# Kernel optimization log

Measured on AMD Instinct MI355X. Metric: run time of the kernel, lower is better.

The kernel has to match this reference:

```python
import jax, jax.numpy as jnp
import numpy as np

H = 1024          # hidden_size
C = 4             # residual_channels
RH = 16           # residual_heads
HS = H // RH      # head_size for residual (64)
DR = 8            # delta_rank
M = 4096          # mlp_size
NH = 16           # attention heads
HD = H // NH      # attention head dim (64)
A_SIZE = (C - 1) * RH   # 48
B_SIZE = C * RH         # 64
EPS = 1e-5
SSM_EPS = 1e-5


def rat_read(res, W, gamma, beta, num_outputs):
    # res: [b,l,H*C]; W: [H, num_outputs, C] (Conv1d groups=H)
    b, l, _ = res.shape
    x = res.reshape(b, l, H, C)
    y = jnp.einsum('blhc,hoc->bloh', x, W)            # [b,l,o,H]
    mu = y.mean(-1, keepdims=True)
    var = y.var(-1, keepdims=True)
    yn = (y - mu) * jax.lax.rsqrt(var + EPS)          # GroupNorm: each group = one output
    yn = yn * gamma.reshape(num_outputs, H) + beta.reshape(num_outputs, H)
    return yn.reshape(b, l, num_outputs * H)


def rope(x, pos):
    # x: [b,l,NH,HD], pos: [b,l]
    half = HD // 2
    inv = 1.0 / (10000.0 ** (jnp.arange(half, dtype=jnp.float32) / half))
    ang = pos.astype(jnp.float32)[..., None] * inv    # [b,l,half]
    cos = jnp.cos(ang)[:, :, None, :]
    sin = jnp.sin(ang)[:, :, None, :]
    x1, x2 = x[..., :half], x[..., half:]
    return jnp.concatenate([x1 * cos - x2 * sin, x2 * cos + x1 * sin], axis=-1)


def attention(qkv_in, qkv_w, pos):
    # qkv_in: [b,l,3H]; qkv_w: [3,H,H] (grouped 1x1 conv = 3 independent linears)
    b, l, _ = qkv_in.shape
    q, k, v = jnp.split(qkv_in, 3, axis=-1)
    q = jnp.einsum('bli,oi->blo', q, qkv_w[0]).reshape(b, l, NH, HD)
    k = jnp.einsum('bli,oi->blo', k, qkv_w[1]).reshape(b, l, NH, HD)
    v = jnp.einsum('bli,oi->blo', v, qkv_w[2]).reshape(b, l, NH, HD)
    q = rope(q, pos)
    k = rope(k, pos)
    scores = jnp.einsum('bqhd,bkhd->bhqk', q, k) / np.sqrt(HD).astype(np.float32)
    mask = jnp.tril(jnp.ones((l, l), dtype=bool))
    scores = jnp.where(mask, scores, jnp.float32(-1e30))
    p = jax.nn.softmax(scores, axis=-1)
    o = jnp.einsum('bhqk,bkhd->bqhd', p, v)
    return o.reshape(b, l, H)  # get_o is identity (no output proj)


def rat_write(res, y, wod_w, wab_w, wab_b, du_w, du_b):
    # res: [b,l,H*C], y: [b,l,y_size]
    b, l, _ = res.shape
    o_d = y @ wod_w.T                                 # [b,l,H+DR]
    A_B = y @ wab_w.T + wab_b                         # [b,l,A+B]
    out = o_d[..., :H]
    delta_low = o_d[..., H:]
    A_logit = A_B[..., :A_SIZE]
    B_proj = A_B[..., A_SIZE:2 * A_SIZE]
    B_skip = A_B[..., 2 * A_SIZE:]
    delta = jax.nn.softplus(delta_low @ du_w.T + du_b)  # [b,l,H]
    hs = res.reshape(b, l, HS, RH, C)
    out = out.reshape(b, l, HS, RH, 1)
    delta = delta.reshape(b, l, HS, RH, 1)
    A_logit = A_logit.reshape(b, l, 1, RH, C - 1)
    B_proj = B_proj.reshape(b, l, 1, RH, C - 1)
    B_skip = B_skip.reshape(b, l, 1, RH, 1)
    A_neg = -jax.nn.softplus(A_logit)
    A_bar = jnp.exp(delta * A_neg)
    B_bar = (A_bar - 1.0) / (A_neg - SSM_EPS) * B_proj
    B_bar_skip = delta * B_skip
    A_full = jnp.concatenate([A_bar, jnp.ones_like(A_bar[..., :1])], axis=-1)
    B_full = jnp.concatenate([B_bar, B_bar_skip], axis=-1)
    return (hs * A_full + out * B_full).reshape(b, l, H * C)


def layer_forward(hidden_states, position_ids, attn_read_w, attn_read_g, attn_read_b,
                  qkv_w, attn_wod_w, attn_wab_w, attn_wab_b, attn_du_w, attn_du_b,
                  mlp_read_w, mlp_read_g, mlp_read_b, mlp_in_w,
                  mlp_wod_w, mlp_wab_w, mlp_wab_b, mlp_du_w, mlp_du_b):
    qkv_in = rat_read(hidden_states, attn_read_w, attn_read_g, attn_read_b, 3)
    attn_out = attention(qkv_in, qkv_w, position_ids)
    hidden_states = rat_write(hidden_states, attn_out, attn_wod_w, attn_wab_w,
                              attn_wab_b, attn_du_w, attn_du_b)
    mlp_in = rat_read(hidden_states, mlp_read_w, mlp_read_g, mlp_read_b, 2)
    g_in, u_in = mlp_in[..., :H], mlp_in[..., H:]
    gate = jnp.einsum('bli,oi->blo', g_in, mlp_in_w[0])
    up = jnp.einsum('bli,oi->blo', u_in, mlp_in_w[1])
    mlp_out = jax.nn.silu(gate) * up                  # [b,l,M]
    hidden_states = rat_write(hidden_states, mlp_out, mlp_wod_w, mlp_wab_w,
                              mlp_wab_b, mlp_du_w, mlp_du_b)
    return hidden_states


def setup_inputs() -> dict:
    key = jax.random.key(0)
    ks = jax.random.split(key, 20)
    B, L = 2, 2048
    s = 0.02
    return {
        'hidden_states': jax.random.normal(ks[0], (B, L, H * C), jnp.float32),
        'position_ids': jnp.tile(jnp.arange(L, dtype=jnp.int64), (B, 1)),
        'attn_read_w': jax.random.normal(ks[1], (H, 3, C), jnp.float32) / np.sqrt(C).astype(np.float32),
        'attn_read_g': jnp.ones((3 * H,), jnp.float32),
        'attn_read_b': jnp.zeros((3 * H,), jnp.float32),
        'qkv_w': jax.random.normal(ks[2], (3, H, H), jnp.float32) * s,
        'attn_wod_w': jax.random.normal(ks[3], (H + DR, H), jnp.float32) * s,
        'attn_wab_w': jax.random.normal(ks[4], (A_SIZE + B_SIZE, H), jnp.float32) * s,
        'attn_wab_b': jax.random.normal(ks[5], (A_SIZE + B_SIZE,), jnp.float32) * s,
        'attn_du_w': jax.random.normal(ks[6], (H, DR), jnp.float32) * s,
        'attn_du_b': jax.random.normal(ks[7], (H,), jnp.float32) * s,
        'mlp_read_w': jax.random.normal(ks[8], (H, 2, C), jnp.float32) / np.sqrt(C).astype(np.float32),
        'mlp_read_g': jnp.ones((2 * H,), jnp.float32),
        'mlp_read_b': jnp.zeros((2 * H,), jnp.float32),
        'mlp_in_w': jax.random.normal(ks[9], (2, M, H), jnp.float32) * s,
        'mlp_wod_w': jax.random.normal(ks[10], (H + DR, M), jnp.float32) * s,
        'mlp_wab_w': jax.random.normal(ks[11], (A_SIZE + B_SIZE, M), jnp.float32) * s,
        'mlp_wab_b': jax.random.normal(ks[12], (A_SIZE + B_SIZE,), jnp.float32) * s,
        'mlp_du_w': jax.random.normal(ks[13], (H, DR), jnp.float32) * s,
        'mlp_du_b': jax.random.normal(ks[14], (H,), jnp.float32) * s,
    }


def reference(hidden_states, position_ids, attn_read_w, attn_read_g, attn_read_b,
              qkv_w, attn_wod_w, attn_wab_w, attn_wab_b, attn_du_w, attn_du_b,
              mlp_read_w, mlp_read_g, mlp_read_b, mlp_in_w,
              mlp_wod_w, mlp_wab_w, mlp_wab_b, mlp_du_w, mlp_du_b):
    return layer_forward(hidden_states, position_ids, attn_read_w, attn_read_g,
                         attn_read_b, qkv_w, attn_wod_w, attn_wab_w, attn_wab_b,
                         attn_du_w, attn_du_b, mlp_read_w, mlp_read_g, mlp_read_b,
                         mlp_in_w, mlp_wod_w, mlp_wab_w, mlp_wab_b, mlp_du_w, mlp_du_b)
```

## Files before the change

kernel.cpp:

```cpp
#include <hip/hip_runtime.h>
#include <hip/hip_bf16.h>
#include <math.h>
#include <stdint.h>


constexpr int NTOK = 4096;

typedef __attribute__((ext_vector_type(8))) short short8_t;
typedef __attribute__((ext_vector_type(4))) float f32x4;

__device__ __forceinline__ ushort f2bf(float f) {
    union { float f; uint32_t u; } v; v.f = f;
    uint32_t r = v.u + 0x7fffu + ((v.u >> 16) & 1u);
    return (ushort)(r >> 16);
}
__device__ __forceinline__ float bf2f(ushort b) {
    union { uint32_t u; float f; } v; v.u = ((uint32_t)b) << 16;
    return v.f;
}
__device__ __forceinline__ uint32_t pack2(float lo, float hi) {
    union { __hip_bfloat162 h; uint32_t u; } v;
    v.h = __float22bfloat162_rn(make_float2(lo, hi));
    return v.u;
}
__device__ __forceinline__ float softplus_f(float x) {
    return (x > 20.0f) ? x : log1pf(expf(x));
}

__device__ __forceinline__ void gload_lds16(const void* g, void* l) {
    __builtin_amdgcn_global_load_lds(
        (const __attribute__((address_space(1))) uint32_t*)g,
        (__attribute__((address_space(3))) uint32_t*)l,
        16, 0, 0);
}

__global__ __launch_bounds__(256) void convert_flat_kernel(
    const float* __restrict__ src, ushort* __restrict__ dst)
{
    const size_t i = ((size_t)blockIdx.x * 256 + threadIdx.x) * 8;
    const float4 a = *(const float4*)(src + i);
    const float4 b = *(const float4*)(src + i + 4);
    union { ushort u[8]; uint4 v; } o;
    o.u[0] = f2bf(a.x); o.u[1] = f2bf(a.y); o.u[2] = f2bf(a.z); o.u[3] = f2bf(a.w);
    o.u[4] = f2bf(b.x); o.u[5] = f2bf(b.y); o.u[6] = f2bf(b.z); o.u[7] = f2bf(b.w);
    *(uint4*)(dst + i) = o.v;
}

__global__ __launch_bounds__(256) void rope_tab_kernel(float2* __restrict__ tab)
{
    const int idx = blockIdx.x * 256 + threadIdx.x;
    const int i = idx & 31;
    const int pos = idx >> 5;
    const float inv = expf(-(float)i * (9.210340371976184f / 32.0f));
    float s, c;
    sincosf((float)pos * inv, &s, &c);
    tab[idx] = make_float2(c, s);
}

__global__ __launch_bounds__(256) void build_comb_kernel(
    const float* __restrict__ wod, const float* __restrict__ wab,
    ushort* __restrict__ dst, int K)
{
    const size_t i = ((size_t)blockIdx.x * 256 + threadIdx.x) * 8;
    const int row = (int)(i / (size_t)K);
    const int col = (int)(i % (size_t)K);
    const float* src = nullptr;
    if (row < 1024)      src = wod + (size_t)row * K + col;
    else if (row < 1136) src = wab + (size_t)(row - 1024) * K + col;
    else if (row < 1144) src = wod + (size_t)(1024 + row - 1136) * K + col;
    union { ushort u[8]; uint4 v; } o;
    if (src) {
        const float4 a = *(const float4*)(src);
        const float4 b = *(const float4*)(src + 4);
        o.u[0] = f2bf(a.x); o.u[1] = f2bf(a.y); o.u[2] = f2bf(a.z); o.u[3] = f2bf(a.w);
        o.u[4] = f2bf(b.x); o.u[5] = f2bf(b.y); o.u[6] = f2bf(b.z); o.u[7] = f2bf(b.w);
    } else {
        o.v = make_uint4(0, 0, 0, 0);
    }
    *(uint4*)(dst + i) = o.v;
}

template <int NO>
__global__ __launch_bounds__(256) void rat_read_kernel(
    const float* __restrict__ res, const float* __restrict__ W,
    const float* __restrict__ gamma, const float* __restrict__ beta,
    ushort* __restrict__ out)
{
    const int t = blockIdx.x;
    const int tid = threadIdx.x;
    const float* rp = res + (size_t)t * 4096;
    float y[4][NO];
#pragma unroll
    for (int i = 0; i < 4; ++i) {
        const int h = tid + 256 * i;
        const float4 x = *(const float4*)(rp + h * 4);
#pragma unroll
        for (int o = 0; o < NO; ++o) {
            const float4 w = *(const float4*)(W + ((size_t)h * NO + o) * 4);
            y[i][o] = x.x * w.x + x.y * w.y + x.z * w.z + x.w * w.w;
        }
    }
    __shared__ float red[4][NO][2];
    const int lane = tid & 63, wid = tid >> 6;
#pragma unroll
    for (int o = 0; o < NO; ++o) {
        float s = 0.f, ss = 0.f;
#pragma unroll
        for (int i = 0; i < 4; ++i) { s += y[i][o]; ss += y[i][o] * y[i][o]; }
        for (int off = 32; off > 0; off >>= 1) {
            s += __shfl_down(s, off);
            ss += __shfl_down(ss, off);
        }
        if (lane == 0) { red[wid][o][0] = s; red[wid][o][1] = ss; }
    }
    __syncthreads();
    float mu[NO], rs[NO];
#pragma unroll
    for (int o = 0; o < NO; ++o) {
        const float s  = red[0][o][0] + red[1][o][0] + red[2][o][0] + red[3][o][0];
        const float ss = red[0][o][1] + red[1][o][1] + red[2][o][1] + red[3][o][1];
        const float m = s * (1.0f / 1024.0f);
        const float v = ss * (1.0f / 1024.0f) - m * m;
        mu[o] = m;
        rs[o] = rsqrtf(v + 1e-5f);
    }
    ushort* op = out + (size_t)t * (NO * 1024);
#pragma unroll
    for (int i = 0; i < 4; ++i) {
        const int h = tid + 256 * i;
#pragma unroll
        for (int o = 0; o < NO; ++o) {
            op[o * 1024 + h] = f2bf((y[i][o] - mu[o]) * rs[o] * gamma[o * 1024 + h] + beta[o * 1024 + h]);
        }
    }
}

template <int EPI>
__global__ __launch_bounds__(256) void mfma_gemm_kernel(
    const ushort* __restrict__ A, int lda,
    const ushort* __restrict__ W, int ldw,
    void* __restrict__ Cp, int ldc,
    const ushort* __restrict__ U,
    int Kblk)
{
    __shared__ ushort lds[2][2][128 * 32];
    const int tid = threadIdx.x;
    const int nwg = gridDim.x * gridDim.y;
    const int gy = gridDim.y;
    const int id = blockIdx.y * gridDim.x + blockIdx.x;
    const int swz = (id & 7) * (nwg >> 3) + (id >> 3);
    const int bm = (swz / gy) * 128;
    const int bo = (swz % gy) * 128;

    const int w = tid >> 6, l = tid & 63;
    const int lq = l & 15, lg = l >> 4;
    const int wr = (w >> 1) * 64, wc = (w & 1) * 64;

    f32x4 acc[4][4];
#pragma unroll
    for (int i = 0; i < 4; ++i)
#pragma unroll
        for (int j = 0; j < 4; ++j) acc[i][j] = (f32x4){0.f, 0.f, 0.f, 0.f};

    const int srow = w * 32 + (l >> 2);
    const int schunk = (l & 3) ^ ((l >> 3) & 3);
    const ushort* Ag = A + (size_t)(bm + srow) * lda + (size_t)blockIdx.z * Kblk + schunk * 8;
    const ushort* Wg = W + (size_t)(bo + srow) * ldw + (size_t)blockIdx.z * Kblk + schunk * 8;
    const size_t lda16 = (size_t)16 * lda, ldw16 = (size_t)16 * ldw;

    const int nt = Kblk >> 5;
    int cur = 0;
#pragma unroll
    for (int i = 0; i < 2; ++i) {
        gload_lds16(Ag + i * lda16, &lds[0][0][(w * 32 + i * 16) * 32]);
        gload_lds16(Wg + i * ldw16, &lds[0][1][(w * 32 + i * 16) * 32]);
    }
    __syncthreads();
    for (int t = 0; t < nt; ++t) {
        if (t + 1 < nt) {
            const int k0 = (t + 1) * 32;
#pragma unroll
            for (int i = 0; i < 2; ++i) {
                gload_lds16(Ag + k0 + i * lda16, &lds[cur ^ 1][0][(w * 32 + i * 16) * 32]);
                gload_lds16(Wg + k0 + i * ldw16, &lds[cur ^ 1][1][(w * 32 + i * 16) * 32]);
            }
        }
        short8_t af[4], bf[4];
#pragma unroll
        for (int mf = 0; mf < 4; ++mf) {
            const int ra = wr + mf * 16 + lq;
            af[mf] = *(const short8_t*)&lds[cur][0][ra * 32 + ((lg ^ ((ra >> 1) & 3)) * 8)];
            const int rb = wc + mf * 16 + lq;
            bf[mf] = *(const short8_t*)&lds[cur][1][rb * 32 + ((lg ^ ((rb >> 1) & 3)) * 8)];
        }
        __builtin_amdgcn_s_setprio(1);
#pragma unroll
        for (int mf = 0; mf < 4; ++mf)
#pragma unroll
            for (int nf = 0; nf < 4; ++nf)
                acc[mf][nf] = __builtin_amdgcn_mfma_f32_16x16x32_bf16(
                    af[mf], bf[nf], acc[mf][nf], 0, 0, 0);
        __builtin_amdgcn_s_setprio(0);
        __syncthreads();
        cur ^= 1;
    }

    ushort* eb = &lds[0][0][0] + w * 4096;
#pragma unroll
    for (int mf = 0; mf < 4; ++mf)
#pragma unroll
        for (int r = 0; r < 4; ++r)
#pragma unroll
            for (int nf = 0; nf < 4; ++nf) {
                const int rl = mf * 16 + lg * 4 + r;
                const int cl = nf * 16 + lq;
                eb[rl * 64 + cl] = f2bf(acc[mf][nf][r]);
            }
#pragma unroll
    for (int p = 0; p < 8; ++p) {
        const int rl = p * 8 + (l >> 3);
        const int cl = (l & 7) * 8;
        const uint4 v = *(const uint4*)&eb[rl * 64 + cl];
        ushort* dst = (ushort*)Cp + ((size_t)blockIdx.z * NTOK + bm + wr + rl) * ldc + bo + wc + cl;
        *(uint4*)dst = v;
    }
}

template <int EPI>
__global__ __launch_bounds__(512) void gemm256_kernel(
    const ushort* __restrict__ A, int lda,
    const ushort* __restrict__ W, int ldw,
    ushort* __restrict__ Cp, int ldc,
    const ushort* __restrict__ U, int K)
{
    __shared__ ushort lds[32768];
    const int tid = threadIdx.x;
    const int nwg = gridDim.x * gridDim.y;
    const int gy = gridDim.y;
    const int id = blockIdx.y * gridDim.x + blockIdx.x;
    const int swz = (id & 7) * (nwg >> 3) + (id >> 3);
    const int bm = (swz / gy) * 128;
    const int bo = (swz % gy) * 256;

    const int w = tid >> 6, l = tid & 63;
    const int lq = l & 15, lg = l >> 4;
    const int wrow = (w >> 2) * 64, wcol = (w & 3) * 64;

    f32x4 acc[4][4];
#pragma unroll
    for (int i = 0; i < 4; ++i)
#pragma unroll
        for (int j = 0; j < 4; ++j) acc[i][j] = (f32x4){0.f, 0.f, 0.f, 0.f};

    const int schunk = (l & 3) ^ ((l >> 3) & 3);
    const ushort* Ab = A + (size_t)(bm + (l >> 2)) * lda + schunk * 8;
    const ushort* Wb = W + (size_t)(bo + (l >> 2)) * ldw + schunk * 8;

    const int nt = K >> 5;
    int cur = 0;
#pragma unroll
    for (int i = 0; i < 3; ++i) {
        const int c = w * 3 + i;
        const ushort* src = (c < 8) ? Ab + (size_t)(c * 16) * lda
                                    : Wb + (size_t)((c - 8) * 16) * ldw;
        gload_lds16(src, &lds[c * 512]);
    }
    __syncthreads();
    for (int t = 0; t < nt; ++t) {
        if (t + 1 < nt) {
            const int k0 = (t + 1) * 32;
#pragma unroll
            for (int i = 0; i < 3; ++i) {
                const int c = w * 3 + i;
                const ushort* src = (c < 8) ? Ab + (size_t)(c * 16) * lda + k0
                                            : Wb + (size_t)((c - 8) * 16) * ldw + k0;
                gload_lds16(src, &lds[(cur ^ 1) * 12288 + c * 512]);
            }
        }
        short8_t af[4], bf[4];
#pragma unroll
        for (int mf = 0; mf < 4; ++mf) {
            const int ra = wrow + mf * 16 + lq;
            af[mf] = *(const short8_t*)&lds[cur * 12288 + ra * 32 + ((lg ^ ((ra >> 1) & 3)) * 8)];
            const int rb = wcol + mf * 16 + lq;
            bf[mf] = *(const short8_t*)&lds[cur * 12288 + (128 + rb) * 32 + ((lg ^ ((rb >> 1) & 3)) * 8)];
        }
        __builtin_amdgcn_s_setprio(1);
#pragma unroll
        for (int mf = 0; mf < 4; ++mf)
#pragma unroll
            for (int nf = 0; nf < 4; ++nf)
                acc[mf][nf] = __builtin_amdgcn_mfma_f32_16x16x32_bf16(
                    af[mf], bf[nf], acc[mf][nf], 0, 0, 0);
        __builtin_amdgcn_s_setprio(0);
        __syncthreads();
        cur ^= 1;
    }

    ushort* eb = lds + w * 4096;
#pragma unroll
    for (int mf = 0; mf < 4; ++mf)
#pragma unroll
        for (int r = 0; r < 4; ++r)
#pragma unroll
            for (int nf = 0; nf < 4; ++nf) {
                const int rl = mf * 16 + lg * 4 + r;
                const int cl = nf * 16 + lq;
                eb[rl * 64 + cl] = f2bf(acc[mf][nf][r]);
            }
#pragma unroll
    for (int p = 0; p < 8; ++p) {
        const int rl = p * 8 + (l >> 3);
        const int cl = (l & 7) * 8;
        const uint4 v = *(const uint4*)&eb[rl * 64 + cl];
        const size_t row = bm + wrow + rl;
        const size_t col = bo + wcol + cl;
        if (EPI == 1) {
            *(uint4*)(Cp + row * ldc + col) = v;
        } else {
            const uint4 uv = *(const uint4*)(U + row * ldc + col);
            union { uint4 v; ushort u[8]; } g, uu, o;
            g.v = v; uu.v = uv;
#pragma unroll
            for (int e = 0; e < 8; ++e) {
                const float gf = bf2f(g.u[e]);
                o.u[e] = f2bf(gf / (1.0f + __expf(-gf)) * bf2f(uu.u[e]));
            }
            *(uint4*)(Cp + row * ldc + col) = o.v;
        }
    }
}

__global__ __launch_bounds__(256) void qkv_gemm_kernel(
    const ushort* __restrict__ Ain, const ushort* __restrict__ Wall,
    const float2* __restrict__ rtab,
    ushort* __restrict__ Qb, ushort* __restrict__ Kb, ushort* __restrict__ Vt)
{
    __shared__ ushort lds[2][2][128 * 32];
    const int tid = threadIdx.x;
    const int z = blockIdx.z;
    const int nwg = gridDim.x * gridDim.y;
    const int gy = gridDim.y;
    const int id = blockIdx.y * gridDim.x + blockIdx.x;
    const int swz = (id & 7) * (nwg >> 3) + (id >> 3);
    const int bm = (swz / gy) * 128;
    const int bo = (swz % gy) * 128;

    const int w = tid >> 6, l = tid & 63;
    const int lq = l & 15, lg = l >> 4;
    const int wr = (w >> 1) * 64, wc = (w & 1) * 64;

    f32x4 acc[4][4];
#pragma unroll
    for (int i = 0; i < 4; ++i)
#pragma unroll
        for (int j = 0; j < 4; ++j) acc[i][j] = (f32x4){0.f, 0.f, 0.f, 0.f};

    const int srow = w * 32 + (l >> 2);
    const int schunk = (l & 3) ^ ((l >> 3) & 3);
    const ushort* Ag = Ain + z * 1024 + (size_t)(bm + srow) * 3072 + schunk * 8;
    const ushort* Wg = Wall + (size_t)z * 1048576 + (size_t)(bo + srow) * 1024 + schunk * 8;
    const size_t lda16 = (size_t)16 * 3072, ldw16 = (size_t)16 * 1024;

    int cur = 0;
#pragma unroll
    for (int i = 0; i < 2; ++i) {
        gload_lds16(Ag + i * lda16, &lds[0][0][(w * 32 + i * 16) * 32]);
        gload_lds16(Wg + i * ldw16, &lds[0][1][(w * 32 + i * 16) * 32]);
    }
    __syncthreads();
    for (int t = 0; t < 32; ++t) {
        if (t + 1 < 32) {
            const int k0 = (t + 1) * 32;
#pragma unroll
            for (int i = 0; i < 2; ++i) {
                gload_lds16(Ag + k0 + i * lda16, &lds[cur ^ 1][0][(w * 32 + i * 16) * 32]);
                gload_lds16(Wg + k0 + i * ldw16, &lds[cur ^ 1][1][(w * 32 + i * 16) * 32]);
            }
        }
        short8_t af[4], bf[4];
#pragma unroll
        for (int mf = 0; mf < 4; ++mf) {
            const int ra = wr + mf * 16 + lq;
            af[mf] = *(const short8_t*)&lds[cur][0][ra * 32 + ((lg ^ ((ra >> 1) & 3)) * 8)];
            const int rb = wc + mf * 16 + lq;
            bf[mf] = *(const short8_t*)&lds[cur][1][rb * 32 + ((lg ^ ((rb >> 1) & 3)) * 8)];
        }
        __builtin_amdgcn_s_setprio(1);
#pragma unroll
        for (int mf = 0; mf < 4; ++mf)
#pragma unroll
            for (int nf = 0; nf < 4; ++nf)
                acc[mf][nf] = __builtin_amdgcn_mfma_f32_16x16x32_bf16(
                    af[mf], bf[nf], acc[mf][nf], 0, 0, 0);
        __builtin_amdgcn_s_setprio(0);
        __syncthreads();
        cur ^= 1;
    }

    if (z < 2) {
        ushort* Out = z ? Kb : Qb;
        const float scale = z ? 1.0f : 0.18033688f;
        const int cbase = bo + wc;
#pragma unroll
        for (int mf = 0; mf < 4; ++mf)
#pragma unroll
            for (int r = 0; r < 4; ++r) {
                const int row = bm + wr + mf * 16 + lg * 4 + r;
                const int pos = row & 2047;
#pragma unroll
                for (int nf = 0; nf < 2; ++nf) {
                    const int i = nf * 16 + lq;
                    const float2 cs = rtab[pos * 32 + i];
                    const float x1 = acc[mf][nf][r];
                    const float x2 = acc[mf][nf + 2][r];
                    Out[(size_t)row * 1024 + cbase + i]      = f2bf((x1 * cs.x - x2 * cs.y) * scale);
                    Out[(size_t)row * 1024 + cbase + i + 32] = f2bf((x2 * cs.x + x1 * cs.y) * scale);
                }
            }
    } else {
        ushort* eb = &lds[0][0][0] + w * 4096;
#pragma unroll
        for (int mf = 0; mf < 4; ++mf)
#pragma unroll
            for (int r = 0; r < 4; ++r)
#pragma unroll
                for (int nf = 0; nf < 4; ++nf) {
                    const int rl = mf * 16 + lg * 4 + r;
                    const int cl = nf * 16 + lq;
                    eb[cl * 64 + rl] = f2bf(acc[mf][nf][r]);
                }
#pragma unroll
        for (int p = 0; p < 8; ++p) {
            const int rl = p * 8 + (l >> 3);
            const int cl = (l & 7) * 8;
            const uint4 v = *(const uint4*)&eb[rl * 64 + cl];
            *(uint4*)(Vt + (size_t)(bo + wc + rl) * NTOK + bm + wr + cl) = v;
        }
    }
}

__global__ __launch_bounds__(512) void attn_mfma_kernel(
    const ushort* __restrict__ Qb, const ushort* __restrict__ Kb,
    const ushort* __restrict__ Vt, ushort* __restrict__ atno)
{
    __shared__ ushort Ks[2][2][64 * 64];
    __shared__ ushort Vs[2][2][64 * 64];
    const int bh = blockIdx.y;
    const int b = bh >> 4, h = bh & 15;
    const int tid = threadIdx.x;
    const int w = tid >> 6, l = tid & 63;
    const int g = l >> 4, t = l & 15;
    const int tok0 = b * 2048;
    const int hoff = h * 64;

    const int srow = w * 8 + (l >> 3);
    const int schunk = (l & 7) ^ (l >> 3);
    const ushort* Kg = Kb + (size_t)(tok0 + srow) * 1024 + hoff + schunk * 8;
    const ushort* Vg = Vt + (size_t)(hoff + srow) * NTOK + tok0 + schunk * 8;
    const int ldsbase = w * 512;

    const int srcA = ((g & 1) * 2) * 16 + t;
    const int srcB = srcA + 16;
    const bool hiSel = (g >> 1) != 0;

    const int bx = (bh & 16) ? (15 - (int)blockIdx.x) : (int)blockIdx.x;
    const int q0 = 31 - bx;
    const int q1 = bx;
    const int nt0 = (q0 + 2) >> 1;
    const int qi = w >> 2;
    const int wq = w & 3;
    const int qb = qi ? q1 : q0;
    const int ntq = (qb + 2) >> 1;
    const int qabs = qb * 64 + wq * 16 + t;

    short8_t qf[2];
#pragma unroll
    for (int ks = 0; ks < 2; ++ks)
        qf[ks] = *(const short8_t*)(Qb + (size_t)(tok0 + qabs) * 1024 + hoff + ks * 32 + g * 8);

    float m_run = -3.0e38f, l_run = 0.0f;
    f32x4 oacc[4];
#pragma unroll
    for (int nf = 0; nf < 4; ++nf) oacc[nf] = (f32x4){0.f, 0.f, 0.f, 0.f};

#pragma unroll
    for (int hf = 0; hf < 2; ++hf) {
        gload_lds16(Kg + (size_t)(hf * 64) * 1024, &Ks[0][hf][ldsbase]);
        gload_lds16(Vg + hf * 64, &Vs[0][hf][ldsbase]);
    }
    __syncthreads();

    int buf = 0;
    for (int kt = 0; kt < nt0; ++kt) {
        if (kt + 1 < nt0) {
            const int nk = (kt + 1) * 128;
#pragma unroll
            for (int hf = 0; hf < 2; ++hf) {
                gload_lds16(Kg + (size_t)(nk + hf * 64) * 1024, &Ks[buf ^ 1][hf][ldsbase]);
                gload_lds16(Vg + nk + hf * 64, &Vs[buf ^ 1][hf][ldsbase]);
            }
        }
        if (kt < ntq) {
            f32x4 sa[2][4];
#pragma unroll
            for (int hf = 0; hf < 2; ++hf)
#pragma unroll
                for (int mf = 0; mf < 4; ++mf) sa[hf][mf] = (f32x4){0.f, 0.f, 0.f, 0.f};
            __builtin_amdgcn_s_setprio(1);
#pragma unroll
            for (int hf = 0; hf < 2; ++hf)
#pragma unroll
                for (int ks = 0; ks < 2; ++ks) {
                    const int jc = ks * 4 + g;
#pragma unroll
                    for (int mf = 0; mf < 4; ++mf) {
                        const short8_t kf = *(const short8_t*)&Ks[buf][hf][(mf * 16 + t) * 64 + ((jc ^ (t & 7)) * 8)];
                        sa[hf][mf] = __builtin_amdgcn_mfma_f32_16x16x32_bf16(kf, qf[ks], sa[hf][mf], 0, 0, 0);
                    }
                }
            __builtin_amdgcn_s_setprio(0);

            float p[2][4][4];
            float mloc = -3.0e38f;
            const bool lastTile = (kt == ntq - 1);
#pragma unroll
            for (int hf = 0; hf < 2; ++hf)
#pragma unroll
                for (int mf = 0; mf < 4; ++mf)
#pragma unroll
                    for (int r = 0; r < 4; ++r) {
                        float s = sa[hf][mf][r];
                        if (lastTile && (kt * 128 + hf * 64 + mf * 16 + g * 4 + r) > qabs) s = -3.0e38f;
                        p[hf][mf][r] = s;
                        mloc = fmaxf(mloc, s);
                    }
            mloc = fmaxf(mloc, __shfl_xor(mloc, 16));
            mloc = fmaxf(mloc, __shfl_xor(mloc, 32));
            const float mnew = fmaxf(m_run, mloc);
            float lsum = 0.f;
#pragma unroll
            for (int hf = 0; hf < 2; ++hf)
#pragma unroll
                for (int mf = 0; mf < 4; ++mf)
#pragma unroll
                    for (int r = 0; r < 4; ++r) {
                        const float e = exp2f(p[hf][mf][r] - mnew);
                        p[hf][mf][r] = e;
                        lsum += e;
                    }
            lsum += __shfl_xor(lsum, 16);
            lsum += __shfl_xor(lsum, 32);
            const float fac = exp2f(m_run - mnew);
            l_run = l_run * fac + lsum;
            m_run = mnew;
#pragma unroll
            for (int r = 0; r < 4; ++r) {
                const float fr = __shfl(fac, g * 4 + r);
#pragma unroll
                for (int nf = 0; nf < 4; ++nf) oacc[nf][r] *= fr;
            }
#pragma unroll
            for (int hf = 0; hf < 2; ++hf) {
                uint32_t pk[4][2];
#pragma unroll
                for (int mf = 0; mf < 4; ++mf) {
                    pk[mf][0] = pack2(p[hf][mf][0], p[hf][mf][1]);
                    pk[mf][1] = pack2(p[hf][mf][2], p[hf][mf][3]);
                }
#pragma unroll
                for (int ks = 0; ks < 2; ++ks) {
                    const uint32_t a00 = __shfl(pk[2 * ks][0], srcA);
                    const uint32_t a01 = __shfl(pk[2 * ks][1], srcA);
                    const uint32_t a10 = __shfl(pk[2 * ks + 1][0], srcA);
                    const uint32_t a11 = __shfl(pk[2 * ks + 1][1], srcA);
                    const uint32_t b00 = __shfl(pk[2 * ks][0], srcB);
                    const uint32_t b01 = __shfl(pk[2 * ks][1], srcB);
                    const uint32_t b10 = __shfl(pk[2 * ks + 1][0], srcB);
                    const uint32_t b11 = __shfl(pk[2 * ks + 1][1], srcB);
                    union { uint32_t u[4]; short8_t v; } pa;
                    pa.u[0] = hiSel ? a10 : a00;
                    pa.u[1] = hiSel ? a11 : a01;
                    pa.u[2] = hiSel ? b10 : b00;
                    pa.u[3] = hiSel ? b11 : b01;
                    const int jc = ks * 4 + g;
                    __builtin_amdgcn_s_setprio(1);
#pragma unroll
                    for (int nf = 0; nf < 4; ++nf) {
                        const short8_t vf = *(const short8_t*)&Vs[buf][hf][(nf * 16 + t) * 64 + ((jc ^ (t & 7)) * 8)];
                        oacc[nf] = __builtin_amdgcn_mfma_f32_16x16x32_bf16(pa.v, vf, oacc[nf], 0, 0, 0);
                    }
                    __builtin_amdgcn_s_setprio(0);
                }
            }
        }
        __syncthreads();
        buf ^= 1;
    }

    const float inv = 1.0f / l_run;
#pragma unroll
    for (int r = 0; r < 4; ++r) {
        const float ir = __shfl(inv, g * 4 + r);
        const int orow = tok0 + qb * 64 + wq * 16 + g * 4 + r;
#pragma unroll
        for (int nf = 0; nf < 4; ++nf)
            atno[(size_t)orow * 1024 + hoff + nf * 16 + t] = f2bf(oacc[nf][r] * ir);
    }
}

template <int FUSE_READ>
__global__ __launch_bounds__(256) void rat_write_kernel(
    const float* __restrict__ res, const ushort* __restrict__ part,
    const float* __restrict__ wab_b, const float* __restrict__ du_w,
    const float* __restrict__ du_b, float* __restrict__ out,
    const float* __restrict__ Wr, const float* __restrict__ gamma,
    const float* __restrict__ beta, ushort* __restrict__ mlp_in)
{
    const int t = blockIdx.x;
    const int tid = threadIdx.x;
    const size_t zs = (size_t)NTOK * 1152;
    const ushort* p0 = part + (size_t)t * 1152;
    __shared__ float sAB[112];
    __shared__ float sdl[8];
    __shared__ float sA2[48];
    __shared__ float sBf[48];
    __shared__ float sBs[16];
    if (tid < 112)
        sAB[tid] = bf2f(p0[1024 + tid]) + bf2f(p0[zs + 1024 + tid])
                 + bf2f(p0[2 * zs + 1024 + tid]) + bf2f(p0[3 * zs + 1024 + tid]) + wab_b[tid];
    if (tid >= 128 && tid < 136) {
        const int j = tid - 128;
        sdl[j] = bf2f(p0[1136 + j]) + bf2f(p0[zs + 1136 + j])
               + bf2f(p0[2 * zs + 1136 + j]) + bf2f(p0[3 * zs + 1136 + j]);
    }
    __syncthreads();
    if (tid < 48) {
        const float Aneg = -softplus_f(sAB[tid]);
        sA2[tid] = Aneg * 1.4426950408889634f;
        sBf[tid] = sAB[48 + tid] / (Aneg - 1e-5f);
    } else if (tid >= 64 && tid < 80) {
        sBs[tid - 64] = sAB[96 + (tid - 64)];
    }
    __syncthreads();
    const float* rp = res + (size_t)t * 4096;
    float* op = out + (size_t)t * 4096;
    float y[4][2];
#pragma unroll
    for (int ii = 0; ii < 4; ++ii) {
        const int hh = tid + 256 * ii;
        const int rh = hh & 15;
        const float4 w0 = *(const float4*)(du_w + hh * 8);
        const float4 w1 = *(const float4*)(du_w + hh * 8 + 4);
        float dacc = du_b[hh];
        dacc += sdl[0] * w0.x + sdl[1] * w0.y + sdl[2] * w0.z + sdl[3] * w0.w;
        dacc += sdl[4] * w1.x + sdl[5] * w1.y + sdl[6] * w1.z + sdl[7] * w1.w;
        const float delta = softplus_f(dacc);
        const float oh = bf2f(p0[hh]) + bf2f(p0[zs + hh]) + bf2f(p0[2 * zs + hh]) + bf2f(p0[3 * zs + hh]);
        const float4 hs = *(const float4*)(rp + hh * 4);
        const float r4[4] = {hs.x, hs.y, hs.z, hs.w};
        float o4[4];
#pragma unroll
        for (int c = 0; c < 3; ++c) {
            const float Abar = exp2f(delta * sA2[rh * 3 + c]);
            o4[c] = r4[c] * Abar + oh * (Abar - 1.0f) * sBf[rh * 3 + c];
        }
        o4[3] = r4[3] + oh * (delta * sBs[rh]);
        *(float4*)(op + hh * 4) = make_float4(o4[0], o4[1], o4[2], o4[3]);
        if (FUSE_READ) {
#pragma unroll
            for (int o = 0; o < 2; ++o) {
                const float4 w = *(const float4*)(Wr + ((size_t)hh * 2 + o) * 4);
                y[ii][o] = o4[0] * w.x + o4[1] * w.y + o4[2] * w.z + o4[3] * w.w;
            }
        }
    }
    if (FUSE_READ) {
        __shared__ float red[4][2][2];
        const int lane = tid & 63, wid = tid >> 6;
#pragma unroll
        for (int o = 0; o < 2; ++o) {
            float s = 0.f, ss = 0.f;
#pragma unroll
            for (int i = 0; i < 4; ++i) { s += y[i][o]; ss += y[i][o] * y[i][o]; }
            for (int off = 32; off > 0; off >>= 1) {
                s += __shfl_down(s, off);
                ss += __shfl_down(ss, off);
            }
            if (lane == 0) { red[wid][o][0] = s; red[wid][o][1] = ss; }
        }
        __syncthreads();
        float mu[2], rs[2];
#pragma unroll
        for (int o = 0; o < 2; ++o) {
            const float s  = red[0][o][0] + red[1][o][0] + red[2][o][0] + red[3][o][0];
            const float ss = red[0][o][1] + red[1][o][1] + red[2][o][1] + red[3][o][1];
            const float m = s * (1.0f / 1024.0f);
            const float v = ss * (1.0f / 1024.0f) - m * m;
            mu[o] = m;
            rs[o] = rsqrtf(v + 1e-5f);
        }
        ushort* mp = mlp_in + (size_t)t * 2048;
#pragma unroll
        for (int i = 0; i < 4; ++i) {
            const int h = tid + 256 * i;
#pragma unroll
            for (int o = 0; o < 2; ++o)
                mp[o * 1024 + h] = f2bf((y[i][o] - mu[o]) * rs[o] * gamma[o * 1024 + h] + beta[o * 1024 + h]);
        }
    }
}

extern "C" void kernel_launch(void* const* d_in, const int* in_sizes, int n_in,
                              void* d_out, int out_size, void* d_ws, size_t ws_size,
                              hipStream_t stream)
{
    const float* hidden      = (const float*)d_in[0];
    const float* attn_read_w = (const float*)d_in[2];
    const float* attn_read_g = (const float*)d_in[3];
    const float* attn_read_b = (const float*)d_in[4];
    const float* qkv_w       = (const float*)d_in[5];
    const float* attn_wod_w  = (const float*)d_in[6];
    const float* attn_wab_w  = (const float*)d_in[7];
    const float* attn_wab_b  = (const float*)d_in[8];
    const float* attn_du_w   = (const float*)d_in[9];
    const float* attn_du_b   = (const float*)d_in[10];
    const float* mlp_read_w  = (const float*)d_in[11];
    const float* mlp_read_g  = (const float*)d_in[12];
    const float* mlp_read_b  = (const float*)d_in[13];
    const float* mlp_in_w    = (const float*)d_in[14];
    const float* mlp_wod_w   = (const float*)d_in[15];
    const float* mlp_wab_w   = (const float*)d_in[16];
    const float* mlp_wab_b   = (const float*)d_in[17];
    const float* mlp_du_w    = (const float*)d_in[18];
    const float* mlp_du_b    = (const float*)d_in[19];
    float* out = (float*)d_out;
    char* wsb = (char*)d_ws;
    const size_t N = NTOK;

    ushort* qkv_wb  = (ushort*)(wsb + 0);
    ushort* wcombA  = (ushort*)(wsb + 6291456);
    ushort* mlpin_b = (ushort*)(wsb + 8650752);
    ushort* wcombM  = (ushort*)(wsb + 25427968);
    float2* rtab    = (float2*)(wsb + 34865152);
    char* R1 = wsb + 35389440;
    char* R2 = wsb + 60555264;
    ushort* qkv_in = (ushort*)R1;
    ushort* mlp_in = (ushort*)R1;
    ushort* Qb   = (ushort*)R2;
    ushort* Kb   = (ushort*)(R2 + 8388608);
    ushort* atno = (ushort*)(R2 + 16777216);
    ushort* Vt   = (ushort*)(R2 + 33554432);
    ushort* pA   = (ushort*)(R2 + 25165824);
    ushort* upb  = (ushort*)R2;
    ushort* up_  = (ushort*)(R2 + 33554432);
    ushort* pM   = (ushort*)(R2 + 33554432);

    convert_flat_kernel<<<1536, 256, 0, stream>>>(qkv_w, qkv_wb);
    convert_flat_kernel<<<4096, 256, 0, stream>>>(mlp_in_w, mlpin_b);
    build_comb_kernel<<<576, 256, 0, stream>>>(attn_wod_w, attn_wab_w, wcombA, 1024);
    build_comb_kernel<<<2304, 256, 0, stream>>>(mlp_wod_w, mlp_wab_w, wcombM, 4096);
    rope_tab_kernel<<<256, 256, 0, stream>>>(rtab);

    rat_read_kernel<3><<<N, 256, 0, stream>>>(hidden, attn_read_w, attn_read_g, attn_read_b, qkv_in);

    qkv_gemm_kernel<<<dim3(32, 8, 3), 256, 0, stream>>>(qkv_in, qkv_wb, rtab, Qb, Kb, Vt);

    attn_mfma_kernel<<<dim3(16, 32), 512, 0, stream>>>(Qb, Kb, Vt, atno);

    mfma_gemm_kernel<4><<<dim3(32, 9, 4), 256, 0, stream>>>(atno, 1024, wcombA, 1024, pA, 1152, nullptr, 256);

    rat_write_kernel<1><<<N, 256, 0, stream>>>(hidden, pA, attn_wab_b, attn_du_w, attn_du_b, out,
                                               mlp_read_w, mlp_read_g, mlp_read_b, mlp_in);

    gemm256_kernel<1><<<dim3(32, 16), 512, 0, stream>>>(mlp_in + 1024, 2048, mlpin_b + 4194304, 1024, up_, 4096, nullptr, 1024);
    gemm256_kernel<2><<<dim3(32, 16), 512, 0, stream>>>(mlp_in, 2048, mlpin_b, 1024, upb, 4096, up_, 1024);

    mfma_gemm_kernel<4><<<dim3(32, 9, 4), 256, 0, stream>>>(upb, 4096, wcombM, 4096, pM, 1152, nullptr, 1024);

    rat_write_kernel<0><<<N, 256, 0, stream>>>(out, pM, mlp_wab_b, mlp_du_w, mlp_du_b, out,
                                               nullptr, nullptr, nullptr, nullptr);
}
```

Before: 374.6 us.

## Restructure attention to one query tile per block with 64-key tiles

The attention kernel no longer pairs two query tiles per 512-thread block sharing 128-key K/V tiles. Each 256-thread block now handles a single 64-row query tile over 64-key tiles, and the grid doubles. Block order is reversed for half of the heads to balance the causal workload. This removes waste from warps idling while their partner tile still runs, and halves shared memory per block, at the cost of more blocks, more barriers per key and no K/V sharing between query tiles.

```diff
diff --git a/kernel.cpp b/kernel.cpp
--- a/kernel.cpp
+++ b/kernel.cpp
@@ -440,12 +440,12 @@
     }
 }
 
-__global__ __launch_bounds__(512) void attn_mfma_kernel(
+__global__ __launch_bounds__(256) void attn_mfma_kernel(
     const ushort* __restrict__ Qb, const ushort* __restrict__ Kb,
     const ushort* __restrict__ Vt, ushort* __restrict__ atno)
 {
-    __shared__ ushort Ks[2][2][64 * 64];
-    __shared__ ushort Vs[2][2][64 * 64];
+    __shared__ ushort Ks[2][64 * 64];
+    __shared__ ushort Vs[2][64 * 64];
     const int bh = blockIdx.y;
     const int b = bh >> 4, h = bh & 15;
     const int tid = threadIdx.x;
@@ -454,25 +454,18 @@
     const int tok0 = b * 2048;
     const int hoff = h * 64;
 
-    const int srow = w * 8 + (l >> 3);
+    const int srow = w * 16 + (l >> 3);
     const int schunk = (l & 7) ^ (l >> 3);
     const ushort* Kg = Kb + (size_t)(tok0 + srow) * 1024 + hoff + schunk * 8;
     const ushort* Vg = Vt + (size_t)(hoff + srow) * NTOK + tok0 + schunk * 8;
-    const int ldsbase = w * 512;
 
     const int srcA = ((g & 1) * 2) * 16 + t;
     const int srcB = srcA + 16;
     const bool hiSel = (g >> 1) != 0;
 
-    const int bx = (bh & 16) ? (15 - (int)blockIdx.x) : (int)blockIdx.x;
-    const int q0 = 31 - bx;
-    const int q1 = bx;
-    const int nt0 = (q0 + 2) >> 1;
-    const int qi = w >> 2;
-    const int wq = w & 3;
-    const int qb = qi ? q1 : q0;
-    const int ntq = (qb + 2) >> 1;
-    const int qabs = qb * 64 + wq * 16 + t;
+    const int qb = ((bh >> 3) & 1) ? (31 - (int)blockIdx.x) : (int)blockIdx.x;
+    const int nt = qb + 1;
+    const int qabs = qb * 64 + w * 16 + t;
 
     short8_t qf[2];
 #pragma unroll
@@ -485,114 +478,101 @@
     for (int nf = 0; nf < 4; ++nf) oacc[nf] = (f32x4){0.f, 0.f, 0.f, 0.f};
 
 #pragma unroll
-    for (int hf = 0; hf < 2; ++hf) {
-        gload_lds16(Kg + (size_t)(hf * 64) * 1024, &Ks[0][hf][ldsbase]);
-        gload_lds16(Vg + hf * 64, &Vs[0][hf][ldsbase]);
+    for (int i = 0; i < 2; ++i) {
+        gload_lds16(Kg + (size_t)(i * 8) * 1024, &Ks[0][(w * 16 + i * 8) * 64]);
+        gload_lds16(Vg + (size_t)(i * 8) * NTOK, &Vs[0][(w * 16 + i * 8) * 64]);
     }
     __syncthreads();
 
     int buf = 0;
-    for (int kt = 0; kt < nt0; ++kt) {
-        if (kt + 1 < nt0) {
-            const int nk = (kt + 1) * 128;
-#pragma unroll
-            for (int hf = 0; hf < 2; ++hf) {
-                gload_lds16(Kg + (size_t)(nk + hf * 64) * 1024, &Ks[buf ^ 1][hf][ldsbase]);
-                gload_lds16(Vg + nk + hf * 64, &Vs[buf ^ 1][hf][ldsbase]);
-            }
-        }
-        if (kt < ntq) {
-            f32x4 sa[2][4];
-#pragma unroll
-            for (int hf = 0; hf < 2; ++hf)
-#pragma unroll
-                for (int mf = 0; mf < 4; ++mf) sa[hf][mf] = (f32x4){0.f, 0.f, 0.f, 0.f};
+    for (int kt = 0; kt < nt; ++kt) {
+        if (kt + 1 < nt) {
+            const int nk = (kt + 1) * 64;
+#pragma unroll
+            for (int i = 0; i < 2; ++i) {
+                gload_lds16(Kg + (size_t)(nk + i * 8) * 1024, &Ks[buf ^ 1][(w * 16 + i * 8) * 64]);
+                gload_lds16(Vg + nk + (size_t)(i * 8) * NTOK, &Vs[buf ^ 1][(w * 16 + i * 8) * 64]);
+            }
+        }
+        f32x4 sa[4];
+#pragma unroll
+        for (int mf = 0; mf < 4; ++mf) sa[mf] = (f32x4){0.f, 0.f, 0.f, 0.f};
+        __builtin_amdgcn_s_setprio(1);
+#pragma unroll
+        for (int ks = 0; ks < 2; ++ks) {
+            const int jc = ks * 4 + g;
+#pragma unroll
+            for (int mf = 0; mf < 4; ++mf) {
+                const short8_t kf = *(const short8_t*)&Ks[buf][(mf * 16 + t) * 64 + ((jc ^ (t & 7)) * 8)];
+                sa[mf] = __builtin_amdgcn_mfma_f32_16x16x32_bf16(kf, qf[ks], sa[mf], 0, 0, 0);
+            }
+        }
+        __builtin_amdgcn_s_setprio(0);
+
+        float p[4][4];
+        float mloc = -3.0e38f;
+        const bool lastTile = (kt == nt - 1);
+#pragma unroll
+        for (int mf = 0; mf < 4; ++mf)
+#pragma unroll
+            for (int r = 0; r < 4; ++r) {
+                float s = sa[mf][r];
+                if (lastTile && (kt * 64 + mf * 16 + g * 4 + r) > qabs) s = -3.0e38f;
+                p[mf][r] = s;
+                mloc = fmaxf(mloc, s);
+            }
+        mloc = fmaxf(mloc, __shfl_xor(mloc, 16));
+        mloc = fmaxf(mloc, __shfl_xor(mloc, 32));
+        const float mnew = fmaxf(m_run, mloc);
+        float lsum = 0.f;
+#pragma unroll
+        for (int mf = 0; mf < 4; ++mf)
+#pragma unroll
+            for (int r = 0; r < 4; ++r) {
+                const float e = exp2f(p[mf][r] - mnew);
+                p[mf][r] = e;
+                lsum += e;
+            }
+        lsum += __shfl_xor(lsum, 16);
+        lsum += __shfl_xor(lsum, 32);
+        const float fac = exp2f(m_run - mnew);
+        l_run = l_run * fac + lsum;
+        m_run = mnew;
+#pragma unroll
+        for (int r = 0; r < 4; ++r) {
+            const float fr = __shfl(fac, g * 4 + r);
+#pragma unroll
+            for (int nf = 0; nf < 4; ++nf) oacc[nf][r] *= fr;
+        }
+        uint32_t pk[4][2];
+#pragma unroll
+        for (int mf = 0; mf < 4; ++mf) {
+            pk[mf][0] = pack2(p[mf][0], p[mf][1]);
+            pk[mf][1] = pack2(p[mf][2], p[mf][3]);
+        }
+#pragma unroll
+        for (int ks = 0; ks < 2; ++ks) {
+            const uint32_t a00 = __shfl(pk[2 * ks][0], srcA);
+            const uint32_t a01 = __shfl(pk[2 * ks][1], srcA);
+            const uint32_t a10 = __shfl(pk[2 * ks + 1][0], srcA);
+            const uint32_t a11 = __shfl(pk[2 * ks + 1][1], srcA);
+            const uint32_t b00 = __shfl(pk[2 * ks][0], srcB);
+            const uint32_t b01 = __shfl(pk[2 * ks][1], srcB);
+            const uint32_t b10 = __shfl(pk[2 * ks + 1][0], srcB);
+            const uint32_t b11 = __shfl(pk[2 * ks + 1][1], srcB);
+            union { uint32_t u[4]; short8_t v; } pa;
+            pa.u[0] = hiSel ? a10 : a00;
+            pa.u[1] = hiSel ? a11 : a01;
+            pa.u[2] = hiSel ? b10 : b00;
+            pa.u[3] = hiSel ? b11 : b01;
+            const int jc = ks * 4 + g;
             __builtin_amdgcn_s_setprio(1);
 #pragma unroll
-            for (int hf = 0; hf < 2; ++hf)
-#pragma unroll
-                for (int ks = 0; ks < 2; ++ks) {
-                    const int jc = ks * 4 + g;
-#pragma unroll
-                    for (int mf = 0; mf < 4; ++mf) {
-                        const short8_t kf = *(const short8_t*)&Ks[buf][hf][(mf * 16 + t) * 64 + ((jc ^ (t & 7)) * 8)];
-                        sa[hf][mf] = __builtin_amdgcn_mfma_f32_16x16x32_bf16(kf, qf[ks], sa[hf][mf], 0, 0, 0);
-                    }
-                }
+            for (int nf = 0; nf < 4; ++nf) {
+                const short8_t vf = *(const short8_t*)&Vs[buf][(nf * 16 + t) * 64 + ((jc ^ (t & 7)) * 8)];
+                oacc[nf] = __builtin_amdgcn_mfma_f32_16x16x32_bf16(pa.v, vf, oacc[nf], 0, 0, 0);
+            }
             __builtin_amdgcn_s_setprio(0);
-
-            float p[2][4][4];
-            float mloc = -3.0e38f;
-            const bool lastTile = (kt == ntq - 1);
-#pragma unroll
-            for (int hf = 0; hf < 2; ++hf)
-#pragma unroll
-                for (int mf = 0; mf < 4; ++mf)
-#pragma unroll
-                    for (int r = 0; r < 4; ++r) {
-                        float s = sa[hf][mf][r];
-                        if (lastTile && (kt * 128 + hf * 64 + mf * 16 + g * 4 + r) > qabs) s = -3.0e38f;
-                        p[hf][mf][r] = s;
-                        mloc = fmaxf(mloc, s);
-                    }
-            mloc = fmaxf(mloc, __shfl_xor(mloc, 16));
-            mloc = fmaxf(mloc, __shfl_xor(mloc, 32));
-            const float mnew = fmaxf(m_run, mloc);
-            float lsum = 0.f;
-#pragma unroll
-            for (int hf = 0; hf < 2; ++hf)
-#pragma unroll
-                for (int mf = 0; mf < 4; ++mf)
-#pragma unroll
-                    for (int r = 0; r < 4; ++r) {
-                        const float e = exp2f(p[hf][mf][r] - mnew);
-                        p[hf][mf][r] = e;
-                        lsum += e;
-                    }
-            lsum += __shfl_xor(lsum, 16);
-            lsum += __shfl_xor(lsum, 32);
-            const float fac = exp2f(m_run - mnew);
-            l_run = l_run * fac + lsum;
-            m_run = mnew;
-#pragma unroll
-            for (int r = 0; r < 4; ++r) {
-                const float fr = __shfl(fac, g * 4 + r);
-#pragma unroll
-                for (int nf = 0; nf < 4; ++nf) oacc[nf][r] *= fr;
-            }
-#pragma unroll
-            for (int hf = 0; hf < 2; ++hf) {
-                uint32_t pk[4][2];
-#pragma unroll
-                for (int mf = 0; mf < 4; ++mf) {
-                    pk[mf][0] = pack2(p[hf][mf][0], p[hf][mf][1]);
-                    pk[mf][1] = pack2(p[hf][mf][2], p[hf][mf][3]);
-                }
-#pragma unroll
-                for (int ks = 0; ks < 2; ++ks) {
-                    const uint32_t a00 = __shfl(pk[2 * ks][0], srcA);
-                    const uint32_t a01 = __shfl(pk[2 * ks][1], srcA);
-                    const uint32_t a10 = __shfl(pk[2 * ks + 1][0], srcA);
-                    const uint32_t a11 = __shfl(pk[2 * ks + 1][1], srcA);
-                    const uint32_t b00 = __shfl(pk[2 * ks][0], srcB);
-                    const uint32_t b01 = __shfl(pk[2 * ks][1], srcB);
-                    const uint32_t b10 = __shfl(pk[2 * ks + 1][0], srcB);
-                    const uint32_t b11 = __shfl(pk[2 * ks + 1][1], srcB);
-                    union { uint32_t u[4]; short8_t v; } pa;
-                    pa.u[0] = hiSel ? a10 : a00;
-                    pa.u[1] = hiSel ? a11 : a01;
-                    pa.u[2] = hiSel ? b10 : b00;
-                    pa.u[3] = hiSel ? b11 : b01;
-                    const int jc = ks * 4 + g;
-                    __builtin_amdgcn_s_setprio(1);
-#pragma unroll
-                    for (int nf = 0; nf < 4; ++nf) {
-                        const short8_t vf = *(const short8_t*)&Vs[buf][hf][(nf * 16 + t) * 64 + ((jc ^ (t & 7)) * 8)];
-                        oacc[nf] = __builtin_amdgcn_mfma_f32_16x16x32_bf16(pa.v, vf, oacc[nf], 0, 0, 0);
-                    }
-                    __builtin_amdgcn_s_setprio(0);
-                }
-            }
         }
         __syncthreads();
         buf ^= 1;
@@ -602,7 +582,7 @@
 #pragma unroll
     for (int r = 0; r < 4; ++r) {
         const float ir = __shfl(inv, g * 4 + r);
-        const int orow = tok0 + qb * 64 + wq * 16 + g * 4 + r;
+        const int orow = tok0 + qb * 64 + w * 16 + g * 4 + r;
 #pragma unroll
         for (int nf = 0; nf < 4; ++nf)
             atno[(size_t)orow * 1024 + hoff + nf * 16 + t] = f2bf(oacc[nf][r] * ir);
@@ -766,7 +746,7 @@
 
     qkv_gemm_kernel<<<dim3(32, 8, 3), 256, 0, stream>>>(qkv_in, qkv_wb, rtab, Qb, Kb, Vt);
 
-    attn_mfma_kernel<<<dim3(16, 32), 512, 0, stream>>>(Qb, Kb, Vt, atno);
+    attn_mfma_kernel<<<dim3(32, 32), 256, 0, stream>>>(Qb, Kb, Vt, atno);
 
     mfma_gemm_kernel<4><<<dim3(32, 9, 4), 256, 0, stream>>>(atno, 1024, wcombA, 1024, pA, 1152, nullptr, 256);
 
```

After: 379.8 us. About the same (+1.4%).
